# Kernel tuning notes

Hardware: AMD Instinct MI355X
Metric: run time of the kernel (lower is better)

## Reference

```python
import jax, jax.numpy as jnp
import numpy as np

N = 200000
D = 256
B = 512  # fixed num_segments (batch.max()+1 in the torch code)
LN_EPS = 1e-5


def _layernorm(h, gamma, beta):
    mu = jnp.mean(h, axis=-1, keepdims=True)
    var = jnp.var(h, axis=-1, keepdims=True)
    return (h - mu) * jax.lax.rsqrt(var + LN_EPS) * gamma + beta


def setup_inputs() -> dict:
    key = jax.random.key(0)
    ks = jax.random.split(key, 10)
    x = jax.random.normal(ks[0], (N, D), dtype=jnp.float32)
    batch = jnp.sort(jax.random.randint(ks[1], (N,), 0, B)).astype(jnp.int64)
    s = 0.05
    return {
        "x": x,
        "batch": batch,
        "vn_embed": jax.random.normal(ks[2], (1, D), dtype=jnp.float32) * 0.02,
        "W1": jax.random.normal(ks[3], (D, D), dtype=jnp.float32) * s,
        "b1": jnp.zeros((D,), dtype=jnp.float32),
        "g1": jnp.ones((D,), dtype=jnp.float32),
        "be1": jnp.zeros((D,), dtype=jnp.float32),
        "W2": jax.random.normal(ks[4], (D, D), dtype=jnp.float32) * s,
        "b2": jnp.zeros((D,), dtype=jnp.float32),
        "g2": jnp.ones((D,), dtype=jnp.float32),
        "be2": jnp.zeros((D,), dtype=jnp.float32),
        "Wg": jax.random.normal(ks[5], (2 * D, D), dtype=jnp.float32) * s,
        "bg": jnp.zeros((D,), dtype=jnp.float32),
    }


def reference(x, batch, vn_embed, W1, b1, g1, be1, W2, b2, g2, be2, Wg, bg):
    # scatter-mean: per-graph average of node features  [B, D]
    seg_sum = jax.ops.segment_sum(x, batch, num_segments=B)
    cnt = jax.ops.segment_sum(jnp.ones((x.shape[0],), x.dtype), batch, num_segments=B)
    node_agg = seg_sum / jnp.maximum(cnt, 1.0)[:, None]
    # node_to_vn: Linear + GELU(exact) + LayerNorm (dropout = identity at eval)
    vn_update = _layernorm(jax.nn.gelu(node_agg @ W1 + b1, approximate=False), g1, be1)
    vn_state = vn_embed + vn_update  # vn_embed broadcasts [1,D] -> [B,D]
    # gather broadcast back to nodes + vn_to_node MLP
    vn_broadcast = vn_state[batch]  # [N, D]
    node_update = _layernorm(jax.nn.gelu(vn_broadcast @ W2 + b2, approximate=False), g2, be2)
    # sigmoid gate on concat + gated residual
    gate = jax.nn.sigmoid(jnp.concatenate([x, node_update], axis=-1) @ Wg + bg)
    x_out = x + gate * node_update
    return (x_out, vn_state)
```

## Files before the change

### kernel.cpp

```cpp
#include <hip/hip_runtime.h>
#include <hip/hip_bf16.h>
#include <math.h>

#define DIM 256
#define B_SEG 512
#define LN_EPS 1e-5f
#define CHUNK 64

typedef __attribute__((ext_vector_type(8))) short bf16x8;
typedef __attribute__((ext_vector_type(4))) float f32x4;

__device__ __forceinline__ float gelu_exact(float v) {
    return 0.5f * v * (1.0f + erff(v * 0.70710678118654752f));
}

__device__ __forceinline__ unsigned int pack2bf(float a, float b) {
    unsigned int ua = (unsigned int)__bfloat16_as_ushort(__float2bfloat16(a));
    unsigned int ub = (unsigned int)__bfloat16_as_ushort(__float2bfloat16(b));
    return ua | (ub << 16);
}

__device__ __forceinline__ void async16(const void* g, void* l) {
    __builtin_amdgcn_global_load_lds(
        (const __attribute__((address_space(1))) void*)(g),
        (__attribute__((address_space(3))) void*)(l), 16, 0, 0);
}

__global__ __launch_bounds__(256) void k_wprep(const float* __restrict__ Wg,
                                               __hip_bfloat16* __restrict__ Wt2) {
    int k = blockIdx.x;
    int c = threadIdx.x;
    Wt2[((size_t)(k >> 3) << 11) + (c << 3) + (k & 7)] = __float2bfloat16(Wg[(size_t)k * DIM + c]);
}

__global__ __launch_bounds__(256) void k_segsum(const float* __restrict__ x,
                                                const int* __restrict__ batch,
                                                float* __restrict__ sums,
                                                float* __restrict__ cnt,
                                                __hip_bfloat16* __restrict__ xbf,
                                                int n, int emit) {
    int i0 = blockIdx.x * CHUNK;
    if (i0 >= n) return;
    int i1 = min(i0 + CHUNK, n);
    const int t    = threadIdx.x;
    const int lane = t & 63;
    const int d4   = lane * 4;
    const int rg   = t >> 6;

    float4 acc = make_float4(0.f, 0.f, 0.f, 0.f);
    int cur = -1;
    int run = 0;
    for (int i = i0 + rg; i < i1; i += 4) {
        int b = batch[i];
        if (b != cur) {
            if (cur >= 0) {
                atomicAdd(&sums[(size_t)cur * DIM + d4 + 0], acc.x);
                atomicAdd(&sums[(size_t)cur * DIM + d4 + 1], acc.y);
                atomicAdd(&sums[(size_t)cur * DIM + d4 + 2], acc.z);
                atomicAdd(&sums[(size_t)cur * DIM + d4 + 3], acc.w);
                if (d4 == 0) atomicAdd(&cnt[cur], (float)run);
            }
            acc = make_float4(0.f, 0.f, 0.f, 0.f);
            run = 0; cur = b;
        }
        float4 v = *(const float4*)(x + (size_t)i * DIM + d4);
        if (emit) {
            uint2 pk;
            pk.x = pack2bf(v.x, v.y);
            pk.y = pack2bf(v.z, v.w);
            *(uint2*)((char*)xbf + (size_t)i * 512 + ((d4 * 2) ^ ((i & 7) << 4))) = pk;
        }
        acc.x += v.x; acc.y += v.y; acc.z += v.z; acc.w += v.w;
        run++;
    }
    if (cur >= 0) {
        atomicAdd(&sums[(size_t)cur * DIM + d4 + 0], acc.x);
        atomicAdd(&sums[(size_t)cur * DIM + d4 + 1], acc.y);
        atomicAdd(&sums[(size_t)cur * DIM + d4 + 2], acc.z);
        atomicAdd(&sums[(size_t)cur * DIM + d4 + 3], acc.w);
        if (d4 == 0) atomicAdd(&cnt[cur], (float)run);
    }
}

__global__ __launch_bounds__(256) void k_vn(const float* __restrict__ sums,
                                            const float* __restrict__ cnt,
                                            const float* __restrict__ vn_embed,
                                            const float* __restrict__ W1, const float* __restrict__ b1,
                                            const float* __restrict__ g1, const float* __restrict__ be1,
                                            const float* __restrict__ W2, const float* __restrict__ b2,
                                            const float* __restrict__ g2, const float* __restrict__ be2,
                                            const float* __restrict__ Wg, const float* __restrict__ bg,
                                            float* __restrict__ vn_state_out,
                                            float* __restrict__ nu,
                                            float* __restrict__ gpart) {
    __shared__ float sIn[DIM];
    __shared__ float sRed[DIM];
    __shared__ float sRed2[DIM];
    const int b = blockIdx.x;
    const int d = threadIdx.x;

    float c = cnt[b];
    float denom = fmaxf(c, 1.0f);
    sIn[d] = sums[(size_t)b * DIM + d] / denom;
    __syncthreads();

    float h0 = 0.f, h1 = 0.f, h2a = 0.f, h3 = 0.f;
    for (int k = 0; k < DIM; k += 4) {
        h0  = fmaf(sIn[k + 0], W1[(size_t)(k + 0) * DIM + d], h0);
        h1  = fmaf(sIn[k + 1], W1[(size_t)(k + 1) * DIM + d], h1);
        h2a = fmaf(sIn[k + 2], W1[(size_t)(k + 2) * DIM + d], h2a);
        h3  = fmaf(sIn[k + 3], W1[(size_t)(k + 3) * DIM + d], h3);
    }
    float h = gelu_exact(b1[d] + ((h0 + h1) + (h2a + h3)));

    sRed[d] = h; sRed2[d] = h * h;
    __syncthreads();
    for (int s = 128; s > 0; s >>= 1) {
        if (d < s) { sRed[d] += sRed[d + s]; sRed2[d] += sRed2[d + s]; }
        __syncthreads();
    }
    float mu = sRed[0] * (1.0f / DIM);
    float var = fmaxf(sRed2[0] * (1.0f / DIM) - mu * mu, 0.0f);
    float rs = rsqrtf(var + LN_EPS);
    float vnst = vn_embed[d] + ((h - mu) * rs * g1[d] + be1[d]);
    vn_state_out[(size_t)b * DIM + d] = vnst;
    __syncthreads();
    sIn[d] = vnst;
    __syncthreads();

    float g0 = 0.f, g1a = 0.f, g2a = 0.f, g3 = 0.f;
    for (int k = 0; k < DIM; k += 4) {
        g0  = fmaf(sIn[k + 0], W2[(size_t)(k + 0) * DIM + d], g0);
        g1a = fmaf(sIn[k + 1], W2[(size_t)(k + 1) * DIM + d], g1a);
        g2a = fmaf(sIn[k + 2], W2[(size_t)(k + 2) * DIM + d], g2a);
        g3  = fmaf(sIn[k + 3], W2[(size_t)(k + 3) * DIM + d], g3);
    }
    float h2 = gelu_exact(b2[d] + ((g0 + g1a) + (g2a + g3)));

    sRed[d] = h2; sRed2[d] = h2 * h2;
    __syncthreads();
    for (int s = 128; s > 0; s >>= 1) {
        if (d < s) { sRed[d] += sRed[d + s]; sRed2[d] += sRed2[d + s]; }
        __syncthreads();
    }
    float mu2 = sRed[0] * (1.0f / DIM);
    float var2 = fmaxf(sRed2[0] * (1.0f / DIM) - mu2 * mu2, 0.0f);
    float rs2 = rsqrtf(var2 + LN_EPS);
    float nud = (h2 - mu2) * rs2 * g2[d] + be2[d];
    nu[(size_t)b * DIM + d] = nud;
    __syncthreads();
    sIn[d] = nud;
    __syncthreads();

    float p0 = 0.f, p1 = 0.f, p2 = 0.f, p3 = 0.f;
    for (int k = 0; k < DIM; k += 4) {
        p0 = fmaf(sIn[k + 0], Wg[(size_t)(DIM + k + 0) * DIM + d], p0);
        p1 = fmaf(sIn[k + 1], Wg[(size_t)(DIM + k + 1) * DIM + d], p1);
        p2 = fmaf(sIn[k + 2], Wg[(size_t)(DIM + k + 2) * DIM + d], p2);
        p3 = fmaf(sIn[k + 3], Wg[(size_t)(DIM + k + 3) * DIM + d], p3);
    }
    gpart[(size_t)b * DIM + d] = bg[d] + ((p0 + p1) + (p2 + p3));
}

__global__ __launch_bounds__(256, 4) void k_gate_bf(const __hip_bfloat16* __restrict__ xbf,
                                                    const int* __restrict__ batch,
                                                    const __hip_bfloat16* __restrict__ Wt2,
                                                    const float* __restrict__ nu,
                                                    const float* __restrict__ gpart,
                                                    float* __restrict__ xout,
                                                    int n) {
    __shared__ __align__(16) char sA[64 * 512];

    const int tid  = threadIdx.x;
    const int wave = tid >> 6;
    const int lane = tid & 63;
    const int r15  = lane & 15;
    const int kq   = lane >> 4;
    const size_t i0 = (size_t)blockIdx.x * 64;

    const char* gsrc = (const char*)xbf + i0 * 512;
    #pragma unroll
    for (int j = 0; j < 8; ++j)
        async16(gsrc + j * 4096 + tid * 16, sA + j * 4096 + wave * 1024);
    __syncthreads();

    f32x4 acc[4][4];
    #pragma unroll
    for (int m = 0; m < 4; ++m)
        #pragma unroll
        for (int nn = 0; nn < 4; ++nn)
            acc[m][nn] = (f32x4){0.f, 0.f, 0.f, 0.f};

    #pragma unroll
    for (int ks = 0; ks < 8; ++ks) {
        bf16x8 a[4], b[4];
        #pragma unroll
        for (int nn = 0; nn < 4; ++nn) {
            int c = wave * 64 + nn * 16 + r15;
            b[nn] = *(const bf16x8*)(Wt2 + ((size_t)(ks * 4 + kq) << 11) + (c << 3));
        }
        #pragma unroll
        for (int m = 0; m < 4; ++m) {
            int r = m * 16 + r15;
            a[m] = *(const bf16x8*)(sA + r * 512 + ((ks * 64 + kq * 16) ^ ((r & 7) << 4)));
        }
        #pragma unroll
        for (int m = 0; m < 4; ++m)
            #pragma unroll
            for (int nn = 0; nn < 4; ++nn)
                acc[m][nn] = __builtin_amdgcn_mfma_f32_16x16x32_bf16(a[m], b[nn], acc[m][nn], 0, 0, 0);
    }

    #pragma unroll
    for (int m = 0; m < 4; ++m) {
        #pragma unroll
        for (int q = 0; q < 4; ++q) {
            int rr = m * 16 + kq * 4 + q;
            long node = (long)(i0 + rr);
            if (node >= n) continue;
            int bb = batch[node];
            #pragma unroll
            for (int nn = 0; nn < 4; ++nn) {
                int col = wave * 64 + nn * 16 + r15;
                float pre = acc[m][nn][q] + gpart[bb * DIM + col];
                float e = __expf(-pre);
                float gte = __builtin_amdgcn_rcpf(1.0f + e);
                float xres = __bfloat162float(
                    *(const __hip_bfloat16*)(sA + rr * 512 + ((2 * col) ^ ((rr & 7) << 4))));
                xout[(size_t)node * DIM + col] = xres + gte * nu[bb * DIM + col];
            }
        }
    }
}

__global__ __launch_bounds__(256) void k_gate_fp(const float* __restrict__ x,
                                                 const int* __restrict__ batch,
                                                 const __hip_bfloat16* __restrict__ Wt2,
                                                 const float* __restrict__ nu,
                                                 const float* __restrict__ gpart,
                                                 float* __restrict__ xout,
                                                 int n) {
    __shared__ __align__(16) char sA[32 * 512];

    const int tid  = threadIdx.x;
    const int wave = tid >> 6;
    const int lane = tid & 63;
    const int r15  = lane & 15;
    const int kq   = lane >> 4;
    const int i0   = blockIdx.x * 32;

    float4 av0[4], av1[4];
    #pragma unroll
    for (int j = 0; j < 4; ++j) {
        int v = j * 256 + tid;
        int r = v >> 5;
        int k8 = v & 31;
        int node = i0 + r;
        if (node < n) {
            const float* p = x + (size_t)node * DIM + k8 * 8;
            av0[j] = *(const float4*)p;
            av1[j] = *(const float4*)(p + 4);
        } else {
            av0[j] = make_float4(0.f, 0.f, 0.f, 0.f);
            av1[j] = av0[j];
        }
    }
    #pragma unroll
    for (int j = 0; j < 4; ++j) {
        int v = j * 256 + tid;
        int r = v >> 5;
        int k8 = v & 31;
        uint4 pk;
        pk.x = pack2bf(av0[j].x, av0[j].y);
        pk.y = pack2bf(av0[j].z, av0[j].w);
        pk.z = pack2bf(av1[j].x, av1[j].y);
        pk.w = pack2bf(av1[j].z, av1[j].w);
        *(uint4*)(sA + r * 512 + ((k8 * 16) ^ ((r & 7) << 4))) = pk;
    }
    __syncthreads();

    f32x4 acc[2][4];
    #pragma unroll
    for (int m = 0; m < 2; ++m)
        #pragma unroll
        for (int nn = 0; nn < 4; ++nn)
            acc[m][nn] = (f32x4){0.f, 0.f, 0.f, 0.f};

    #pragma unroll
    for (int ks = 0; ks < 8; ++ks) {
        bf16x8 a[2], b[4];
        #pragma unroll
        for (int nn = 0; nn < 4; ++nn) {
            int c = wave * 64 + nn * 16 + r15;
            b[nn] = *(const bf16x8*)(Wt2 + ((size_t)(ks * 4 + kq) << 11) + (c << 3));
        }
        #pragma unroll
        for (int m = 0; m < 2; ++m) {
            int r = m * 16 + r15;
            a[m] = *(const bf16x8*)(sA + r * 512 + ((ks * 64 + kq * 16) ^ ((r & 7) << 4)));
        }
        #pragma unroll
        for (int m = 0; m < 2; ++m)
            #pragma unroll
            for (int nn = 0; nn < 4; ++nn)
                acc[m][nn] = __builtin_amdgcn_mfma_f32_16x16x32_bf16(a[m], b[nn], acc[m][nn], 0, 0, 0);
    }

    #pragma unroll
    for (int m = 0; m < 2; ++m) {
        #pragma unroll
        for (int q = 0; q < 4; ++q) {
            int rr = m * 16 + kq * 4 + q;
            int node = i0 + rr;
            if (node >= n) continue;
            int bb = batch[node];
            #pragma unroll
            for (int nn = 0; nn < 4; ++nn) {
                int col = wave * 64 + nn * 16 + r15;
                float pre = acc[m][nn][q] + gpart[bb * DIM + col];
                float e = __expf(-pre);
                float gte = __builtin_amdgcn_rcpf(1.0f + e);
                float xres = __bfloat162float(
                    *(const __hip_bfloat16*)(sA + rr * 512 + ((2 * col) ^ ((rr & 7) << 4))));
                xout[(size_t)node * DIM + col] = xres + gte * nu[bb * DIM + col];
            }
        }
    }
}

extern "C" void kernel_launch(void* const* d_in, const int* in_sizes, int n_in,
                              void* d_out, int out_size, void* d_ws, size_t ws_size,
                              hipStream_t stream) {
    const float* x        = (const float*)d_in[0];
    const int*   batch    = (const int*)d_in[1];
    const float* vn_embed = (const float*)d_in[2];
    const float* W1  = (const float*)d_in[3];
    const float* b1  = (const float*)d_in[4];
    const float* g1  = (const float*)d_in[5];
    const float* be1 = (const float*)d_in[6];
    const float* W2  = (const float*)d_in[7];
    const float* b2  = (const float*)d_in[8];
    const float* g2  = (const float*)d_in[9];
    const float* be2 = (const float*)d_in[10];
    const float* Wg  = (const float*)d_in[11];
    const float* bg  = (const float*)d_in[12];

    const int n = in_sizes[0] / DIM;

    float* out = (float*)d_out;
    float* xout = out;
    float* vn_state_out = out + (size_t)n * DIM;

    float* ws    = (float*)d_ws;
    float* sums  = ws;
    float* cnt   = sums + (size_t)B_SEG * DIM;
    float* nu    = cnt + B_SEG;
    float* gpart = nu + (size_t)B_SEG * DIM;
    __hip_bfloat16* Wt2 = (__hip_bfloat16*)(gpart + (size_t)B_SEG * DIM);
    __hip_bfloat16* xbf = Wt2 + (size_t)DIM * DIM;

    const size_t base_bytes = ((size_t)B_SEG * DIM * 3 + B_SEG) * 4 + (size_t)DIM * DIM * 2;
    const int nt64 = (n + 63) / 64;
    const size_t need = base_bytes + (size_t)nt64 * 64 * 512;
    const bool use_bf = (ws_size >= need);

    hipMemsetAsync(d_ws, 0, ((size_t)B_SEG * DIM + B_SEG) * sizeof(float), stream);

    k_wprep<<<DIM, DIM, 0, stream>>>(Wg, Wt2);

    int nblk1 = (n + CHUNK - 1) / CHUNK;
    k_segsum<<<nblk1, 256, 0, stream>>>(x, batch, sums, cnt, xbf, n, use_bf ? 1 : 0);

    k_vn<<<B_SEG, 256, 0, stream>>>(sums, cnt, vn_embed,
                                    W1, b1, g1, be1,
                                    W2, b2, g2, be2,
                                    Wg, bg,
                                    vn_state_out, nu, gpart);

    if (use_bf) {
        k_gate_bf<<<nt64, 256, 0, stream>>>(xbf, batch, Wt2, nu, gpart, xout, n);
    } else {
        int nblk3 = (n + 31) / 32;
        k_gate_fp<<<nblk3, 256, 0, stream>>>(x, batch, Wt2, nu, gpart, xout, n);
    }
}
```

Before: 229.4 us.

## Replace atomic segment-sum with binary-searched segment bounds and per-segment reduction

```diff
diff --git a/kernel.cpp b/kernel.cpp
--- a/kernel.cpp
+++ b/kernel.cpp
@@ -5,7 +5,6 @@
 #define DIM 256
 #define B_SEG 512
 #define LN_EPS 1e-5f
-#define CHUNK 64
 
 typedef __attribute__((ext_vector_type(8))) short bf16x8;
 typedef __attribute__((ext_vector_type(4))) float f32x4;
@@ -33,57 +32,76 @@
     Wt2[((size_t)(k >> 3) << 11) + (c << 3) + (k & 7)] = __float2bfloat16(Wg[(size_t)k * DIM + c]);
 }
 
-__global__ __launch_bounds__(256) void k_segsum(const float* __restrict__ x,
-                                                const int* __restrict__ batch,
-                                                float* __restrict__ sums,
-                                                float* __restrict__ cnt,
-                                                __hip_bfloat16* __restrict__ xbf,
-                                                int n, int emit) {
-    int i0 = blockIdx.x * CHUNK;
-    if (i0 >= n) return;
-    int i1 = min(i0 + CHUNK, n);
-    const int t    = threadIdx.x;
-    const int lane = t & 63;
-    const int d4   = lane * 4;
-    const int rg   = t >> 6;
+__global__ __launch_bounds__(256) void k_bounds(const int* __restrict__ batch,
+                                                int* __restrict__ seg_start, int n) {
+    int s = blockIdx.x * 256 + threadIdx.x;
+    if (s > B_SEG) return;
+    int lo = 0, hi = n;
+    while (lo < hi) {
+        int mid = (lo + hi) >> 1;
+        if (batch[mid] < s) lo = mid + 1; else hi = mid;
+    }
+    seg_start[s] = lo;
+}
+
+__global__ __launch_bounds__(256) void k_segsum2(const float* __restrict__ x,
+                                                 const int* __restrict__ seg_start,
+                                                 float* __restrict__ partial,
+                                                 __hip_bfloat16* __restrict__ xbf,
+                                                 int emit) {
+    const int seg  = blockIdx.x >> 1;
+    const int half = blockIdx.x & 1;
+    const int s0 = seg_start[seg], s1 = seg_start[seg + 1];
+    const int hl = (s1 - s0 + 1) >> 1;
+    const int rs = s0 + half * hl;
+    const int re = half ? s1 : (s0 + hl);
+
+    const int wave = threadIdx.x >> 6;
+    const int lane = threadIdx.x & 63;
+    const int dby  = lane * 8;
 
     float4 acc = make_float4(0.f, 0.f, 0.f, 0.f);
-    int cur = -1;
-    int run = 0;
-    for (int i = i0 + rg; i < i1; i += 4) {
-        int b = batch[i];
-        if (b != cur) {
-            if (cur >= 0) {
-                atomicAdd(&sums[(size_t)cur * DIM + d4 + 0], acc.x);
-                atomicAdd(&sums[(size_t)cur * DIM + d4 + 1], acc.y);
-                atomicAdd(&sums[(size_t)cur * DIM + d4 + 2], acc.z);
-                atomicAdd(&sums[(size_t)cur * DIM + d4 + 3], acc.w);
-                if (d4 == 0) atomicAdd(&cnt[cur], (float)run);
+
+    for (int r0 = rs; r0 < re; r0 += 16) {
+        float4 v[4];
+        #pragma unroll
+        for (int jj = 0; jj < 4; ++jj) {
+            int r = r0 + 4 * jj + wave;
+            v[jj] = (r < re) ? *(const float4*)(x + (size_t)r * DIM + lane * 4)
+                             : make_float4(0.f, 0.f, 0.f, 0.f);
+        }
+        __builtin_amdgcn_sched_barrier(0);
+        #pragma unroll
+        for (int jj = 0; jj < 4; ++jj) {
+            int r = r0 + 4 * jj + wave;
+            if (r < re) {
+                if (emit) {
+                    uint2 pk;
+                    pk.x = pack2bf(v[jj].x, v[jj].y);
+                    pk.y = pack2bf(v[jj].z, v[jj].w);
+                    *(uint2*)((char*)xbf + (size_t)r * 512 + (dby ^ ((r & 7) << 4))) = pk;
+                }
+                acc.x += v[jj].x; acc.y += v[jj].y; acc.z += v[jj].z; acc.w += v[jj].w;
             }
-            acc = make_float4(0.f, 0.f, 0.f, 0.f);
-            run = 0; cur = b;
-        }
-        float4 v = *(const float4*)(x + (size_t)i * DIM + d4);
-        if (emit) {
-            uint2 pk;
-            pk.x = pack2bf(v.x, v.y);
-            pk.y = pack2bf(v.z, v.w);
-            *(uint2*)((char*)xbf + (size_t)i * 512 + ((d4 * 2) ^ ((i & 7) << 4))) = pk;
-        }
-        acc.x += v.x; acc.y += v.y; acc.z += v.z; acc.w += v.w;
-        run++;
-    }
-    if (cur >= 0) {
-        atomicAdd(&sums[(size_t)cur * DIM + d4 + 0], acc.x);
-        atomicAdd(&sums[(size_t)cur * DIM + d4 + 1], acc.y);
-        atomicAdd(&sums[(size_t)cur * DIM + d4 + 2], acc.z);
-        atomicAdd(&sums[(size_t)cur * DIM + d4 + 3], acc.w);
-        if (d4 == 0) atomicAdd(&cnt[cur], (float)run);
-    }
-}
-
-__global__ __launch_bounds__(256) void k_vn(const float* __restrict__ sums,
-                                            const float* __restrict__ cnt,
+        }
+    }
+
+    __shared__ float4 red[4][64];
+    red[wave][lane] = acc;
+    __syncthreads();
+    if (wave == 0) {
+        float4 a0 = red[0][lane], a1 = red[1][lane], a2 = red[2][lane], a3 = red[3][lane];
+        float4 t;
+        t.x = (a0.x + a1.x) + (a2.x + a3.x);
+        t.y = (a0.y + a1.y) + (a2.y + a3.y);
+        t.z = (a0.z + a1.z) + (a2.z + a3.z);
+        t.w = (a0.w + a1.w) + (a2.w + a3.w);
+        *(float4*)(partial + ((size_t)half * B_SEG + seg) * DIM + lane * 4) = t;
+    }
+}
+
+__global__ __launch_bounds__(256) void k_vn(const float* __restrict__ partial,
+                                            const int* __restrict__ seg_start,
                                             const float* __restrict__ vn_embed,
                                             const float* __restrict__ W1, const float* __restrict__ b1,
                                             const float* __restrict__ g1, const float* __restrict__ be1,
@@ -99,9 +117,10 @@
     const int b = blockIdx.x;
     const int d = threadIdx.x;
 
-    float c = cnt[b];
-    float denom = fmaxf(c, 1.0f);
-    sIn[d] = sums[(size_t)b * DIM + d] / denom;
+    float cntf = (float)(seg_start[b + 1] - seg_start[b]);
+    float denom = fmaxf(cntf, 1.0f);
+    sIn[d] = (partial[(size_t)b * DIM + d] +
+              partial[(size_t)(B_SEG + b) * DIM + d]) / denom;
     __syncthreads();
 
     float h0 = 0.f, h1 = 0.f, h2a = 0.f, h3 = 0.f;
@@ -233,6 +252,43 @@
     }
 }
 
+__global__ __launch_bounds__(256) void k_segsum_fp(const float* __restrict__ x,
+                                                   const int* __restrict__ batch,
+                                                   float* __restrict__ sums,
+                                                   int n) {
+    const int i0 = blockIdx.x * 64;
+    if (i0 >= n) return;
+    const int t    = threadIdx.x;
+    const int lane = t & 63;
+    const int d4   = lane * 4;
+    const int rg   = t >> 6;
+    float4 acc = make_float4(0.f, 0.f, 0.f, 0.f);
+    int cur = -1;
+    for (int j = 0; j < 16; ++j) {
+        int i = i0 + rg + 4 * j;
+        if (i >= n) break;
+        int b = batch[i];
+        if (b != cur) {
+            if (cur >= 0) {
+                atomicAdd(&sums[(size_t)cur * DIM + d4 + 0], acc.x);
+                atomicAdd(&sums[(size_t)cur * DIM + d4 + 1], acc.y);
+                atomicAdd(&sums[(size_t)cur * DIM + d4 + 2], acc.z);
+                atomicAdd(&sums[(size_t)cur * DIM + d4 + 3], acc.w);
+            }
+            acc = make_float4(0.f, 0.f, 0.f, 0.f);
+            cur = b;
+        }
+        float4 v = *(const float4*)(x + (size_t)i * DIM + d4);
+        acc.x += v.x; acc.y += v.y; acc.z += v.z; acc.w += v.w;
+    }
+    if (cur >= 0) {
+        atomicAdd(&sums[(size_t)cur * DIM + d4 + 0], acc.x);
+        atomicAdd(&sums[(size_t)cur * DIM + d4 + 1], acc.y);
+        atomicAdd(&sums[(size_t)cur * DIM + d4 + 2], acc.z);
+        atomicAdd(&sums[(size_t)cur * DIM + d4 + 3], acc.w);
+    }
+}
+
 __global__ __launch_bounds__(256) void k_gate_fp(const float* __restrict__ x,
                                                  const int* __restrict__ batch,
                                                  const __hip_bfloat16* __restrict__ Wt2,
@@ -241,7 +297,6 @@
                                                  float* __restrict__ xout,
                                                  int n) {
     __shared__ __align__(16) char sA[32 * 512];
-
     const int tid  = threadIdx.x;
     const int wave = tid >> 6;
     const int lane = tid & 63;
@@ -351,27 +406,31 @@
     float* xout = out;
     float* vn_state_out = out + (size_t)n * DIM;
 
-    float* ws    = (float*)d_ws;
-    float* sums  = ws;
-    float* cnt   = sums + (size_t)B_SEG * DIM;
-    float* nu    = cnt + B_SEG;
-    float* gpart = nu + (size_t)B_SEG * DIM;
+    char* wsb = (char*)d_ws;
+    int*   seg_start = (int*)wsb;
+    float* partial   = (float*)(wsb + 4096);
+    float* nu        = partial + (size_t)2 * B_SEG * DIM;
+    float* gpart     = nu + (size_t)B_SEG * DIM;
     __hip_bfloat16* Wt2 = (__hip_bfloat16*)(gpart + (size_t)B_SEG * DIM);
     __hip_bfloat16* xbf = Wt2 + (size_t)DIM * DIM;
 
-    const size_t base_bytes = ((size_t)B_SEG * DIM * 3 + B_SEG) * 4 + (size_t)DIM * DIM * 2;
     const int nt64 = (n + 63) / 64;
+    const size_t base_bytes = 4096 + (size_t)2 * B_SEG * DIM * 4
+                            + (size_t)B_SEG * DIM * 4 * 2 + (size_t)DIM * DIM * 2;
     const size_t need = base_bytes + (size_t)nt64 * 64 * 512;
     const bool use_bf = (ws_size >= need);
 
-    hipMemsetAsync(d_ws, 0, ((size_t)B_SEG * DIM + B_SEG) * sizeof(float), stream);
-
     k_wprep<<<DIM, DIM, 0, stream>>>(Wg, Wt2);
-
-    int nblk1 = (n + CHUNK - 1) / CHUNK;
-    k_segsum<<<nblk1, 256, 0, stream>>>(x, batch, sums, cnt, xbf, n, use_bf ? 1 : 0);
-
-    k_vn<<<B_SEG, 256, 0, stream>>>(sums, cnt, vn_embed,
+    k_bounds<<<3, 256, 0, stream>>>(batch, seg_start, n);
+
+    if (use_bf) {
+        k_segsum2<<<2 * B_SEG, 256, 0, stream>>>(x, seg_start, partial, xbf, 1);
+    } else {
+        hipMemsetAsync(partial, 0, (size_t)2 * B_SEG * DIM * sizeof(float), stream);
+        k_segsum_fp<<<nt64, 256, 0, stream>>>(x, batch, partial, n);
+    }
+
+    k_vn<<<B_SEG, 256, 0, stream>>>(partial, seg_start, vn_embed,
                                     W1, b1, g1, be1,
                                     W2, b2, g2, be2,
                                     Wg, bg,
```

Measured after the change: 197.2 us. 14.0% less time.
